# Performance work log

Measured on AMD Instinct MI355X. Metric: run time of the kernel, lower is better.

Reference implementation:

```python
import jax, jax.numpy as jnp
import numpy as np

D_MODEL = 1024
ADAPT = 128
NUM_LIB = 8
BATCH = 1024


def setup_inputs() -> dict:
    key = jax.random.key(0)
    k_x, k_src, k_tgt, k_w1, k_w2 = jax.random.split(key, 5)
    hidden_states = jax.random.normal(k_x, (BATCH, D_MODEL), dtype=jnp.float32)
    source_library = jax.random.randint(k_src, (BATCH,), 0, NUM_LIB, dtype=jnp.int32)
    target_library = jax.random.randint(k_tgt, (BATCH,), 0, NUM_LIB, dtype=jnp.int32)
    # Stacked translator weights: slot p = src*NUM_LIB + tgt. Diagonal slots
    # (src==tgt) exist for uniform indexing but are masked out (identity path).
    P = NUM_LIB * NUM_LIB
    s1 = 1.0 / np.sqrt(D_MODEL).astype(np.float32)
    s2 = 1.0 / np.sqrt(ADAPT).astype(np.float32)
    W1 = jax.random.normal(k_w1, (P, D_MODEL, ADAPT), dtype=jnp.float32) * s1
    b1 = jnp.zeros((P, ADAPT), dtype=jnp.float32)
    W2 = jax.random.normal(k_w2, (P, ADAPT, D_MODEL), dtype=jnp.float32) * s2
    b2 = jnp.zeros((P, D_MODEL), dtype=jnp.float32)
    return {
        "hidden_states": hidden_states,
        "source_library": source_library,
        "target_library": target_library,
        "W1": W1, "b1": b1, "W2": W2, "b2": b2,
    }


def reference(hidden_states, source_library, target_library, W1, b1, W2, b2):
    # L recovered from stacked expert table [L*L, d, a]
    L = int(np.sqrt(W1.shape[0]))
    pair = source_library * L + target_library  # [B]
    # Per-sample expert weights (grouped-GEMM formulation of the python loop)
    h = jax.nn.relu(jnp.einsum('bd,bda->ba', hidden_states, W1[pair]) + b1[pair])
    y = jnp.einsum('ba,bad->bd', h, W2[pair]) + b2[pair]
    # src == tgt -> identity (original appends hidden_states[i] unchanged)
    same = (source_library == target_library)[:, None]
    return jnp.where(same, hidden_states, y)
```

## Files before the change

### kernel.cpp

```cpp
#include <hip/hip_runtime.h>

#define D_MODEL 1024
#define ADAPT   128
#define NUM_LIB 8
#define BATCH   1024
#define CH      16
#define NSLOT   128

typedef __attribute__((ext_vector_type(8))) short bf16x8;
typedef __attribute__((ext_vector_type(4))) float f32x4;

__device__ __forceinline__ short f2bf(float f) {
  unsigned u = __float_as_uint(f);
  u += 0x7FFFu + ((u >> 16) & 1u);
  return (short)(u >> 16);
}

__global__ __launch_bounds__(1024) void bucket_k(const int* __restrict__ src,
                                                 const int* __restrict__ tgt,
                                                 int* __restrict__ perm,
                                                 int* __restrict__ cpair,
                                                 int* __restrict__ cbase,
                                                 int* __restrict__ cm) {
  __shared__ int cnt[64];
  __shared__ int offs[64];
  __shared__ int pos[64];
  __shared__ int choff[65];
  int t = threadIdx.x;
  if (t < 64) { cnt[t] = 0; pos[t] = 0; }
  __syncthreads();
  int pair = src[t] * NUM_LIB + tgt[t];
  atomicAdd(&cnt[pair], 1);
  __syncthreads();
  if (t == 0) {
    int acc = 0, ch = 0;
    for (int i = 0; i < 64; i++) {
      offs[i] = acc; acc += cnt[i];
      choff[i] = ch; ch += (cnt[i] + CH - 1) / CH;
    }
    choff[64] = ch;
  }
  __syncthreads();
  int sl = atomicAdd(&pos[pair], 1);
  perm[offs[pair] + sl] = t;
  if (t < 64) {
    int nc = (cnt[t] + CH - 1) / CH, c0 = choff[t];
    for (int c = 0; c < nc; c++) {
      cpair[c0 + c] = t;
      cbase[c0 + c] = offs[t] + c * CH;
      cm[c0 + c]    = min(CH, cnt[t] - c * CH);
    }
  } else if (t < 64 + NSLOT) {
    int slotid = t - 64;
    if (slotid >= choff[64]) cpair[slotid] = -1;
  }
}

#define BK     256
#define XS_STR 520
#define WT_STR 264

__global__ __launch_bounds__(256) void gemm1_k(const float* __restrict__ x,
                                               const float* __restrict__ W1,
                                               const int* __restrict__ perm,
                                               const int* __restrict__ cpair,
                                               const int* __restrict__ cbase,
                                               const int* __restrict__ cm,
                                               float* __restrict__ Hp) {
  int slot = blockIdx.x;
  int p = cpair[slot];
  if (p < 0 || (p % 9) == 0) return;
  int m    = cm[slot];
  int base = cbase[slot];
  int a0   = blockIdx.y * 64;
  int kh   = blockIdx.z;
  __shared__ int   rows_s[CH];
  __shared__ short xs[CH * XS_STR];
  __shared__ short wt[64 * WT_STR];
  int t = threadIdx.x;
  if (t < CH) rows_s[t] = perm[base + min(t, m - 1)];
  __syncthreads();
  {
    int s = t & 15, jg = t >> 4;
    const float* xr = x + (size_t)rows_s[s] * D_MODEL + kh * 512 + jg * 32;
    short* xw = xs + s * XS_STR + jg * 32;
#pragma unroll
    for (int i = 0; i < 8; i++) {
      float4 v = *(const float4*)(xr + i * 4);
      short4 o;
      o.x = f2bf(v.x); o.y = f2bf(v.y); o.z = f2bf(v.z); o.w = f2bf(v.w);
      *(short4*)(xw + i * 4) = o;
    }
  }
  int lane = t & 63, wvid = t >> 6, col = lane & 15, quad = lane >> 4;
  f32x4 acc = {0.f, 0.f, 0.f, 0.f};
  int a_st = t & 63, kg = t >> 6;
  for (int r = 0; r < 2; r++) {
    {
      const float* wr = W1 + ((size_t)p * D_MODEL + kh * 512 + r * BK + kg * 64) * ADAPT + a0 + a_st;
      short* ww = wt + a_st * WT_STR + kg * 64;
#pragma unroll
      for (int ii = 0; ii < 8; ii++) {
        bf16x8 o;
#pragma unroll
        for (int i = 0; i < 8; i++) o[i] = f2bf(wr[(ii * 8 + i) * ADAPT]);
        *(bf16x8*)(ww + ii * 8) = o;
      }
    }
    __syncthreads();
#pragma unroll
    for (int kk = 0; kk < 8; kk++) {
      bf16x8 af = *(const bf16x8*)(xs + col * XS_STR + r * BK + kk * 32 + quad * 8);
      bf16x8 bv = *(const bf16x8*)(wt + (wvid * 16 + col) * WT_STR + kk * 32 + quad * 8);
      acc = __builtin_amdgcn_mfma_f32_16x16x32_bf16(af, bv, acc, 0, 0, 0);
    }
    __syncthreads();
  }
  int a = a0 + wvid * 16 + col;
  float* Hb = Hp + (size_t)kh * BATCH * ADAPT;
#pragma unroll
  for (int r = 0; r < 4; r++) {
    int s = quad * 4 + r;
    if (s < m) Hb[(size_t)rows_s[s] * ADAPT + a] = acc[r];
  }
}

#define HS_STR  136
#define WT2_STR 136

__global__ __launch_bounds__(256) void gemm2_k(const float* __restrict__ x,
                                               const float* __restrict__ W2,
                                               const float* __restrict__ b1,
                                               const float* __restrict__ b2,
                                               const int* __restrict__ perm,
                                               const int* __restrict__ cpair,
                                               const int* __restrict__ cbase,
                                               const int* __restrict__ cm,
                                               const float* __restrict__ Hp,
                                               float* __restrict__ out) {
  int slot = blockIdx.x;
  int p = cpair[slot];
  if (p < 0) return;
  int m    = cm[slot];
  int base = cbase[slot];
  int d0   = blockIdx.y * 128;
  __shared__ int rows_s[CH];
  int t = threadIdx.x;
  if (t < CH) rows_s[t] = perm[base + min(t, m - 1)];
  __syncthreads();
  if ((p % 9) == 0) {
    int s = t >> 4, j = t & 15;
    if (s < m) {
      size_t off = (size_t)rows_s[s] * D_MODEL + d0 + j * 8;
      float4 v0 = *(const float4*)(x + off);
      float4 v1 = *(const float4*)(x + off + 4);
      *(float4*)(out + off)     = v0;
      *(float4*)(out + off + 4) = v1;
    }
    return;
  }
  __shared__ short hs[CH * HS_STR];
  __shared__ short wt[128 * WT2_STR];
  {
    int s = t & 15, j = t >> 4;
    size_t ho = (size_t)rows_s[s] * ADAPT + j * 8;
    const float* h0 = Hp + ho;
    const float* h1 = Hp + (size_t)BATCH * ADAPT + ho;
    const float* bb = b1 + (size_t)p * ADAPT + j * 8;
    bf16x8 o;
#pragma unroll
    for (int i = 0; i < 8; i++) o[i] = f2bf(fmaxf(h0[i] + h1[i] + bb[i], 0.f));
    *(bf16x8*)(hs + s * HS_STR + j * 8) = o;
  }
  {
    int dl = t & 127, half = t >> 7;
#pragma unroll
    for (int kgi = 0; kgi < 8; kgi++) {
      int kb = kgi * 16 + half * 8;
      const float* wr = W2 + ((size_t)p * ADAPT + kb) * D_MODEL + d0 + dl;
      bf16x8 o;
#pragma unroll
      for (int i = 0; i < 8; i++) o[i] = f2bf(wr[i * D_MODEL]);
      *(bf16x8*)(wt + dl * WT2_STR + kb) = o;
    }
  }
  __syncthreads();
  int lane = t & 63, wvid = t >> 6, col = lane & 15, quad = lane >> 4;
  f32x4 acc0 = {0.f, 0.f, 0.f, 0.f};
  f32x4 acc1 = {0.f, 0.f, 0.f, 0.f};
#pragma unroll
  for (int kk = 0; kk < 4; kk++) {
    bf16x8 af = *(const bf16x8*)(hs + col * HS_STR + kk * 32 + quad * 8);
    bf16x8 b0 = *(const bf16x8*)(wt + (wvid * 32 + col) * WT2_STR + kk * 32 + quad * 8);
    bf16x8 b1v = *(const bf16x8*)(wt + (wvid * 32 + 16 + col) * WT2_STR + kk * 32 + quad * 8);
    acc0 = __builtin_amdgcn_mfma_f32_16x16x32_bf16(af, b0, acc0, 0, 0, 0);
    acc1 = __builtin_amdgcn_mfma_f32_16x16x32_bf16(af, b1v, acc1, 0, 0, 0);
  }
  int d_a = d0 + wvid * 32 + col;
  int d_b = d_a + 16;
  float bba = b2[(size_t)p * D_MODEL + d_a];
  float bbb = b2[(size_t)p * D_MODEL + d_b];
#pragma unroll
  for (int r = 0; r < 4; r++) {
    int s = quad * 4 + r;
    if (s < m) {
      size_t ro = (size_t)rows_s[s] * D_MODEL;
      out[ro + d_a] = acc0[r] + bba;
      out[ro + d_b] = acc1[r] + bbb;
    }
  }
}

extern "C" void kernel_launch(void* const* d_in, const int* in_sizes, int n_in,
                              void* d_out, int out_size, void* d_ws, size_t ws_size,
                              hipStream_t stream) {
  const float* x   = (const float*)d_in[0];
  const int*   src = (const int*)d_in[1];
  const int*   tgt = (const int*)d_in[2];
  const float* W1  = (const float*)d_in[3];
  const float* b1  = (const float*)d_in[4];
  const float* W2  = (const float*)d_in[5];
  const float* b2  = (const float*)d_in[6];
  float* out = (float*)d_out;

  float* Hp   = (float*)d_ws;
  int* perm   = (int*)(Hp + 2 * (size_t)BATCH * ADAPT);
  int* cpair  = perm + BATCH;
  int* cbase  = cpair + NSLOT;
  int* cmarr  = cbase + NSLOT;

  bucket_k<<<1, 1024, 0, stream>>>(src, tgt, perm, cpair, cbase, cmarr);
  gemm1_k<<<dim3(NSLOT, 2, 2), 256, 0, stream>>>(x, W1, perm, cpair, cbase, cmarr, Hp);
  gemm2_k<<<dim3(NSLOT, 8), 256, 0, stream>>>(x, W2, b1, b2, perm, cpair, cbase, cmarr, Hp, out);
  (void)in_sizes; (void)n_in; (void)out_size; (void)ws_size;
}
```

Measured before the change: 126.4 us.

## Double chunk size to 32 rows per block and use packed bf16 conversion

Raises the rows per expert chunk from 16 to 32 so each block runs two M-tiles of MFMA over the same converted weight tile in both GEMMs. The intent is to halve redundant loading and fp32-to-bf16 conversion of expert weights, which dominates with about 16 samples per pair. It also replaces the manual rounding helper with the HIP packed float2-to-bf16 intrinsic and writes 16-byte vectors. The cost is fewer blocks (96 slots), more padding waste in partially filled chunks, and more registers per thread.

```diff
diff --git a/kernel.cpp b/kernel.cpp
--- a/kernel.cpp
+++ b/kernel.cpp
@@ -1,19 +1,19 @@
 #include <hip/hip_runtime.h>
+#include <hip/hip_bf16.h>
 
 #define D_MODEL 1024
 #define ADAPT   128
 #define NUM_LIB 8
 #define BATCH   1024
-#define CH      16
-#define NSLOT   128
+#define CH      32
+#define NSLOT   96
 
 typedef __attribute__((ext_vector_type(8))) short bf16x8;
 typedef __attribute__((ext_vector_type(4))) float f32x4;
 
-__device__ __forceinline__ short f2bf(float f) {
-  unsigned u = __float_as_uint(f);
-  u += 0x7FFFu + ((u >> 16) & 1u);
-  return (short)(u >> 16);
+__device__ __forceinline__ unsigned pk2(float a, float b) {
+  __hip_bfloat162 h = __float22bfloat162_rn(make_float2(a, b));
+  return *(unsigned*)&h;
 }
 
 __global__ __launch_bounds__(1024) void bucket_k(const int* __restrict__ src,
@@ -81,38 +81,45 @@
   if (t < CH) rows_s[t] = perm[base + min(t, m - 1)];
   __syncthreads();
   {
-    int s = t & 15, jg = t >> 4;
-    const float* xr = x + (size_t)rows_s[s] * D_MODEL + kh * 512 + jg * 32;
-    short* xw = xs + s * XS_STR + jg * 32;
+    int s = t & 31, jg = t >> 5;
+    const float* xr = x + (size_t)rows_s[s] * D_MODEL + kh * 512 + jg * 64;
+    uint4* xw = (uint4*)(xs + s * XS_STR + jg * 64);
 #pragma unroll
     for (int i = 0; i < 8; i++) {
-      float4 v = *(const float4*)(xr + i * 4);
-      short4 o;
-      o.x = f2bf(v.x); o.y = f2bf(v.y); o.z = f2bf(v.z); o.w = f2bf(v.w);
-      *(short4*)(xw + i * 4) = o;
+      float4 v0 = *(const float4*)(xr + i * 8);
+      float4 v1 = *(const float4*)(xr + i * 8 + 4);
+      uint4 o;
+      o.x = pk2(v0.x, v0.y); o.y = pk2(v0.z, v0.w);
+      o.z = pk2(v1.x, v1.y); o.w = pk2(v1.z, v1.w);
+      xw[i] = o;
     }
   }
   int lane = t & 63, wvid = t >> 6, col = lane & 15, quad = lane >> 4;
-  f32x4 acc = {0.f, 0.f, 0.f, 0.f};
+  f32x4 acc0 = {0.f, 0.f, 0.f, 0.f};
+  f32x4 acc1 = {0.f, 0.f, 0.f, 0.f};
   int a_st = t & 63, kg = t >> 6;
   for (int r = 0; r < 2; r++) {
     {
       const float* wr = W1 + ((size_t)p * D_MODEL + kh * 512 + r * BK + kg * 64) * ADAPT + a0 + a_st;
-      short* ww = wt + a_st * WT_STR + kg * 64;
-#pragma unroll
-      for (int ii = 0; ii < 8; ii++) {
-        bf16x8 o;
-#pragma unroll
-        for (int i = 0; i < 8; i++) o[i] = f2bf(wr[(ii * 8 + i) * ADAPT]);
-        *(bf16x8*)(ww + ii * 8) = o;
+      uint4* ww = (uint4*)(wt + a_st * WT_STR + kg * 64);
+#pragma unroll
+      for (int j8 = 0; j8 < 8; j8++) {
+        uint4 o;
+        o.x = pk2(wr[(j8 * 8 + 0) * ADAPT], wr[(j8 * 8 + 1) * ADAPT]);
+        o.y = pk2(wr[(j8 * 8 + 2) * ADAPT], wr[(j8 * 8 + 3) * ADAPT]);
+        o.z = pk2(wr[(j8 * 8 + 4) * ADAPT], wr[(j8 * 8 + 5) * ADAPT]);
+        o.w = pk2(wr[(j8 * 8 + 6) * ADAPT], wr[(j8 * 8 + 7) * ADAPT]);
+        ww[j8] = o;
       }
     }
     __syncthreads();
 #pragma unroll
     for (int kk = 0; kk < 8; kk++) {
-      bf16x8 af = *(const bf16x8*)(xs + col * XS_STR + r * BK + kk * 32 + quad * 8);
-      bf16x8 bv = *(const bf16x8*)(wt + (wvid * 16 + col) * WT_STR + kk * 32 + quad * 8);
-      acc = __builtin_amdgcn_mfma_f32_16x16x32_bf16(af, bv, acc, 0, 0, 0);
+      bf16x8 af0 = *(const bf16x8*)(xs + col * XS_STR + r * BK + kk * 32 + quad * 8);
+      bf16x8 af1 = *(const bf16x8*)(xs + (16 + col) * XS_STR + r * BK + kk * 32 + quad * 8);
+      bf16x8 bv  = *(const bf16x8*)(wt + (wvid * 16 + col) * WT_STR + kk * 32 + quad * 8);
+      acc0 = __builtin_amdgcn_mfma_f32_16x16x32_bf16(af0, bv, acc0, 0, 0, 0);
+      acc1 = __builtin_amdgcn_mfma_f32_16x16x32_bf16(af1, bv, acc1, 0, 0, 0);
     }
     __syncthreads();
   }
@@ -121,7 +128,8 @@
 #pragma unroll
   for (int r = 0; r < 4; r++) {
     int s = quad * 4 + r;
-    if (s < m) Hb[(size_t)rows_s[s] * ADAPT + a] = acc[r];
+    if (s < m)      Hb[(size_t)rows_s[s] * ADAPT + a]      = acc0[r];
+    if (s + 16 < m) Hb[(size_t)rows_s[s + 16] * ADAPT + a] = acc1[r];
   }
 }
 
@@ -149,28 +157,39 @@
   if (t < CH) rows_s[t] = perm[base + min(t, m - 1)];
   __syncthreads();
   if ((p % 9) == 0) {
-    int s = t >> 4, j = t & 15;
+    int s = t >> 3, j = t & 7;
     if (s < m) {
-      size_t off = (size_t)rows_s[s] * D_MODEL + d0 + j * 8;
+      size_t off = (size_t)rows_s[s] * D_MODEL + d0 + j * 16;
       float4 v0 = *(const float4*)(x + off);
       float4 v1 = *(const float4*)(x + off + 4);
-      *(float4*)(out + off)     = v0;
-      *(float4*)(out + off + 4) = v1;
+      float4 v2 = *(const float4*)(x + off + 8);
+      float4 v3 = *(const float4*)(x + off + 12);
+      *(float4*)(out + off)      = v0;
+      *(float4*)(out + off + 4)  = v1;
+      *(float4*)(out + off + 8)  = v2;
+      *(float4*)(out + off + 12) = v3;
     }
     return;
   }
   __shared__ short hs[CH * HS_STR];
   __shared__ short wt[128 * WT2_STR];
   {
-    int s = t & 15, j = t >> 4;
-    size_t ho = (size_t)rows_s[s] * ADAPT + j * 8;
+    int s = t & 31, j = t >> 5;
+    size_t ho = (size_t)rows_s[s] * ADAPT + j * 16;
     const float* h0 = Hp + ho;
     const float* h1 = Hp + (size_t)BATCH * ADAPT + ho;
-    const float* bb = b1 + (size_t)p * ADAPT + j * 8;
-    bf16x8 o;
-#pragma unroll
-    for (int i = 0; i < 8; i++) o[i] = f2bf(fmaxf(h0[i] + h1[i] + bb[i], 0.f));
-    *(bf16x8*)(hs + s * HS_STR + j * 8) = o;
+    const float* bb = b1 + (size_t)p * ADAPT + j * 16;
+    uint4* hw = (uint4*)(hs + s * HS_STR + j * 16);
+#pragma unroll
+    for (int g = 0; g < 2; g++) {
+      float v[8];
+#pragma unroll
+      for (int i = 0; i < 8; i++) v[i] = fmaxf(h0[g * 8 + i] + h1[g * 8 + i] + bb[g * 8 + i], 0.f);
+      uint4 o;
+      o.x = pk2(v[0], v[1]); o.y = pk2(v[2], v[3]);
+      o.z = pk2(v[4], v[5]); o.w = pk2(v[6], v[7]);
+      hw[g] = o;
+    }
   }
   {
     int dl = t & 127, half = t >> 7;
@@ -178,23 +197,30 @@
     for (int kgi = 0; kgi < 8; kgi++) {
       int kb = kgi * 16 + half * 8;
       const float* wr = W2 + ((size_t)p * ADAPT + kb) * D_MODEL + d0 + dl;
-      bf16x8 o;
-#pragma unroll
-      for (int i = 0; i < 8; i++) o[i] = f2bf(wr[i * D_MODEL]);
-      *(bf16x8*)(wt + dl * WT2_STR + kb) = o;
+      uint4 o;
+      o.x = pk2(wr[0 * D_MODEL], wr[1 * D_MODEL]);
+      o.y = pk2(wr[2 * D_MODEL], wr[3 * D_MODEL]);
+      o.z = pk2(wr[4 * D_MODEL], wr[5 * D_MODEL]);
+      o.w = pk2(wr[6 * D_MODEL], wr[7 * D_MODEL]);
+      *(uint4*)(wt + dl * WT2_STR + kb) = o;
     }
   }
   __syncthreads();
   int lane = t & 63, wvid = t >> 6, col = lane & 15, quad = lane >> 4;
-  f32x4 acc0 = {0.f, 0.f, 0.f, 0.f};
-  f32x4 acc1 = {0.f, 0.f, 0.f, 0.f};
+  f32x4 acc00 = {0.f, 0.f, 0.f, 0.f};
+  f32x4 acc01 = {0.f, 0.f, 0.f, 0.f};
+  f32x4 acc10 = {0.f, 0.f, 0.f, 0.f};
+  f32x4 acc11 = {0.f, 0.f, 0.f, 0.f};
 #pragma unroll
   for (int kk = 0; kk < 4; kk++) {
-    bf16x8 af = *(const bf16x8*)(hs + col * HS_STR + kk * 32 + quad * 8);
-    bf16x8 b0 = *(const bf16x8*)(wt + (wvid * 32 + col) * WT2_STR + kk * 32 + quad * 8);
+    bf16x8 af0 = *(const bf16x8*)(hs + col * HS_STR + kk * 32 + quad * 8);
+    bf16x8 af1 = *(const bf16x8*)(hs + (16 + col) * HS_STR + kk * 32 + quad * 8);
+    bf16x8 b0  = *(const bf16x8*)(wt + (wvid * 32 + col) * WT2_STR + kk * 32 + quad * 8);
     bf16x8 b1v = *(const bf16x8*)(wt + (wvid * 32 + 16 + col) * WT2_STR + kk * 32 + quad * 8);
-    acc0 = __builtin_amdgcn_mfma_f32_16x16x32_bf16(af, b0, acc0, 0, 0, 0);
-    acc1 = __builtin_amdgcn_mfma_f32_16x16x32_bf16(af, b1v, acc1, 0, 0, 0);
+    acc00 = __builtin_amdgcn_mfma_f32_16x16x32_bf16(af0, b0,  acc00, 0, 0, 0);
+    acc01 = __builtin_amdgcn_mfma_f32_16x16x32_bf16(af0, b1v, acc01, 0, 0, 0);
+    acc10 = __builtin_amdgcn_mfma_f32_16x16x32_bf16(af1, b0,  acc10, 0, 0, 0);
+    acc11 = __builtin_amdgcn_mfma_f32_16x16x32_bf16(af1, b1v, acc11, 0, 0, 0);
   }
   int d_a = d0 + wvid * 32 + col;
   int d_b = d_a + 16;
@@ -205,8 +231,13 @@
     int s = quad * 4 + r;
     if (s < m) {
       size_t ro = (size_t)rows_s[s] * D_MODEL;
-      out[ro + d_a] = acc0[r] + bba;
-      out[ro + d_b] = acc1[r] + bbb;
+      out[ro + d_a] = acc00[r] + bba;
+      out[ro + d_b] = acc01[r] + bbb;
+    }
+    if (s + 16 < m) {
+      size_t ro = (size_t)rows_s[s + 16] * D_MODEL;
+      out[ro + d_a] = acc10[r] + bba;
+      out[ro + d_b] = acc11[r] + bbb;
     }
   }
 }
```

Result: faster. 122.4 us (-3.2%).
